# Kernel optimization log

Hardware: AMD Instinct MI355X
Metric: run time of the kernel (lower is better)

Reference implementation:

```python
import jax, jax.numpy as jnp
import numpy as np

N_NODES = 100000
N_EDGES = 1600000
IN_DIM = 128
OUT_DIM = 128


def setup_inputs() -> dict:
    key = jax.random.key(0)
    ks = jax.random.split(key, 8)
    x = jax.random.normal(ks[0], (N_NODES, IN_DIM), dtype=jnp.float32)
    one_hot_h = jax.random.normal(ks[1], (N_NODES, OUT_DIM), dtype=jnp.float32)
    # three candidate-op linear transforms (in_dim -> out_dim)
    W0 = jax.random.normal(ks[2], (IN_DIM, OUT_DIM), dtype=jnp.float32) * 0.05
    W1 = jax.random.normal(ks[3], (IN_DIM, OUT_DIM), dtype=jnp.float32) * 0.05
    W2 = jax.random.normal(ks[4], (IN_DIM, OUT_DIM), dtype=jnp.float32) * 0.05
    # sparse mask_matrix in COO form: out[r] += v * H[c]
    mask_rows = jax.random.randint(ks[5], (N_EDGES,), 0, N_NODES, dtype=jnp.int32)
    mask_cols = jax.random.randint(ks[6], (N_EDGES,), 0, N_NODES, dtype=jnp.int32)
    mask_vals = jax.random.uniform(ks[7], (N_EDGES,), dtype=jnp.float32)
    return {"x": x, "one_hot_h": one_hot_h, "W0": W0, "W1": W1, "W2": W2,
            "mask_rows": mask_rows, "mask_cols": mask_cols, "mask_vals": mask_vals}


def reference(x, one_hot_h, W0, W1, W2, mask_rows, mask_cols, mask_vals):
    # Original: sum_k spmm(mask_matrix, op_k(x)) + spmm(mask_matrix, one_hot_h).
    # spmm is linear, so summing per-op outputs pre-aggregation is exact and
    # fuses K spmm launches into one sparse aggregation pass.
    H = x @ W0 + x @ W1 + x @ W2 + one_hot_h              # [N, out_dim]
    gathered = mask_vals[:, None] * H[mask_cols]          # [E, out_dim]
    out = jax.ops.segment_sum(gathered, mask_rows, num_segments=x.shape[0])
    return out
```

## Files before the change

kernel.cpp:

```cpp
#include <hip/hip_runtime.h>
#include <hip/hip_bf16.h>

#define N_NODES 100000
#define N_EDGES 1600000
#define DIM 128

#define NBIN 512
#define RPP  196
#define PCAP 4096
#define P1_BLOCKS 512
#define CHUNK (N_EDGES / P1_BLOCKS)
#define GEMM_BLOCKS 1563

typedef unsigned int uint_t;
typedef unsigned short ushort_t;
typedef float f32x4 __attribute__((ext_vector_type(4)));
typedef __bf16 bf16x8 __attribute__((ext_vector_type(8)));

__device__ inline uint_t f2bf(float f) {
    uint_t u = __float_as_uint(f);
    return (u + 0x7FFFu + ((u >> 16) & 1u)) >> 16;
}
__device__ inline float bf2f(uint_t lo16) { return __uint_as_float(lo16 << 16); }

__global__ __launch_bounds__(256) void wt_init(const float* __restrict__ W0,
                                               const float* __restrict__ W1,
                                               const float* __restrict__ W2,
                                               ushort_t* __restrict__ WT,
                                               int* __restrict__ psize) {
    if (blockIdx.x == 64) {
        int i = threadIdx.x;
        if (i < NBIN / 2) { ((int2*)psize)[i] = make_int2(0, 0); }
        return;
    }
    int i = blockIdx.x * 256 + threadIdx.x;
    int m = i & 127, k = i >> 7;
    float s = W0[k * DIM + m] + W1[k * DIM + m] + W2[k * DIM + m];
    WT[m * DIM + k] = (ushort_t)f2bf(s);
}

#define GROWS 64
#define XSTR 136

__global__ __launch_bounds__(256) void fused_p1_gemm(
        const int* __restrict__ rows, const int* __restrict__ cols,
        const float* __restrict__ vals, int* __restrict__ psize,
        long long* __restrict__ slab,
        const float* __restrict__ x, const float* __restrict__ oh,
        const ushort_t* __restrict__ WT, uint_t* __restrict__ H16) {
    __shared__ __align__(16) char smem[8192 + CHUNK * 8 + CHUNK * 4];

    int role, idx;
    if (blockIdx.x < 2048) {
        int g = blockIdx.x >> 2, sb = blockIdx.x & 3;
        if (sb == 3) { role = 1; idx = g; }
        else         { role = 0; idx = g * 3 + sb; }
    } else {
        role = 0; idx = 1536 + (int)(blockIdx.x - 2048);
    }
    int t = threadIdx.x;

    if (role == 1) {
        int* hist   = (int*)smem;
        int* binoff = hist + NBIN;
        int* resv   = binoff + NBIN;
        int* curs   = resv + NBIN;
        long long* ebuf = (long long*)(smem + 8192);
        int* edest  = (int*)(smem + 8192 + CHUNK * 8);

        int e0 = idx * CHUNK;

        for (int i = t; i < NBIN; i += 256) hist[i] = 0;
        __syncthreads();

        for (int i = t; i < CHUNK; i += 256) {
            int r = rows[e0 + i];
            atomicAdd(&hist[r / RPP], 1);
        }
        __syncthreads();

        if (t < 64) {
            int b = t * 8;
            int v[8]; int s = 0;
#pragma unroll
            for (int k = 0; k < 8; ++k) { v[k] = hist[b + k]; s += v[k]; }
            int incl = s;
#pragma unroll
            for (int d = 1; d < 64; d <<= 1) {
                int o = __shfl_up(incl, d, 64);
                if (t >= d) incl += o;
            }
            int run = incl - s;
#pragma unroll
            for (int k = 0; k < 8; ++k) { binoff[b + k] = run; run += v[k]; }
        }
        __syncthreads();

        for (int i = t; i < NBIN; i += 256) {
            int len = hist[i];
            int r = (len > 0) ? atomicAdd(&psize[i], len) : 0;
            resv[i] = i * PCAP + r;
            curs[i] = binoff[i];
        }
        __syncthreads();

        for (int i = t; i < CHUNK; i += 256) {
            int   r = rows[e0 + i];
            int   c = cols[e0 + i];
            float v = vals[e0 + i];
            int b  = r / RPP;
            int lr = r - b * RPP;
            int pos = atomicAdd(&curs[b], 1);
            uint_t key = ((uint_t)lr << 17) | (uint_t)c;
            ebuf[pos]  = ((long long)__float_as_int(v) << 32) | (long long)key;
            edest[pos] = resv[b] + (pos - binoff[b]);
        }
        __syncthreads();

        for (int i = t; i < CHUNK; i += 256)
            slab[edest[i]] = ebuf[i];
    } else {
        ushort_t* xs = (ushort_t*)smem;

        int wv = t >> 6, l = t & 63;
        int lr = l & 15, kg = l >> 4;
        int lrow = wv * 16 + lr;
        long long base_row = (long long)idx * GROWS;
        long long hr = base_row + lrow;

        const f32x4* xg = (const f32x4*)x;
#pragma unroll
        for (int i = 0; i < 8; ++i) {
            int g = t + i * 256;
            int row = g >> 5, c4 = g & 31;
            long long sr = base_row + row; if (sr >= N_NODES) sr = N_NODES - 1;
            f32x4 v = __builtin_nontemporal_load(xg + sr * 32 + c4);
            ushort_t* d = &xs[row * XSTR + c4 * 4];
            d[0] = (ushort_t)f2bf(v.x); d[1] = (ushort_t)f2bf(v.y);
            d[2] = (ushort_t)f2bf(v.z); d[3] = (ushort_t)f2bf(v.w);
        }
        __syncthreads();

        f32x4 acc[8] = {};
#pragma unroll
        for (int s = 0; s < 4; ++s) {
            bf16x8 b = *(const bf16x8*)&xs[lrow * XSTR + s * 32 + kg * 8];
#pragma unroll
            for (int mt = 0; mt < 8; ++mt) {
                bf16x8 a = *(const bf16x8*)&WT[(mt * 16 + lr) * DIM + s * 32 + kg * 8];
                acc[mt] = __builtin_amdgcn_mfma_f32_16x16x32_bf16(a, b, acc[mt], 0, 0, 0);
            }
        }
        __syncthreads();

        const f32x4* og = (const f32x4*)oh;
#pragma unroll
        for (int i = 0; i < 8; ++i) {
            int g = t + i * 256;
            int row = g >> 5, c4 = g & 31;
            long long sr = base_row + row; if (sr >= N_NODES) sr = N_NODES - 1;
            f32x4 v = __builtin_nontemporal_load(og + sr * 32 + c4);
            ushort_t* d = &xs[row * XSTR + c4 * 4];
            d[0] = (ushort_t)f2bf(v.x); d[1] = (ushort_t)f2bf(v.y);
            d[2] = (ushort_t)f2bf(v.z); d[3] = (ushort_t)f2bf(v.w);
        }
        __syncthreads();

        if (hr < N_NODES) {
#pragma unroll
            for (int mt = 0; mt < 8; ++mt) {
                int c0 = mt * 16 + kg * 4;
                const uint_t* ow = (const uint_t*)&xs[lrow * XSTR + c0];
                uint_t w0 = ow[0], w1 = ow[1];
                float f0 = acc[mt].x + bf2f(w0 & 0xFFFFu);
                float f1 = acc[mt].y + bf2f(w0 >> 16);
                float f2 = acc[mt].z + bf2f(w1 & 0xFFFFu);
                float f3 = acc[mt].w + bf2f(w1 >> 16);
                uint2 pk;
                pk.x = f2bf(f0) | (f2bf(f1) << 16);
                pk.y = f2bf(f2) | (f2bf(f3) << 16);
                *(uint2*)&H16[(size_t)hr * (DIM / 2) + c0 / 2] = pk;
            }
        }
    }
}

__global__ __launch_bounds__(256) void pass2_sort(
        const long long* __restrict__ slab, const int* __restrict__ psize,
        int* __restrict__ off, long long* __restrict__ csr) {
    __shared__ int pb[NBIN + 1];
    __shared__ int cnt[RPP + 1];
    __shared__ int loff[RPP + 1];
    __shared__ int curs[RPP];
    __shared__ long long ebuf[PCAP];

    int p = blockIdx.x, t = threadIdx.x;

    if (t < 64) {
        int b = t * 8;
        int v[8]; int s = 0;
#pragma unroll
        for (int k = 0; k < 8; ++k) { v[k] = min(psize[b + k], PCAP); s += v[k]; }
        int incl = s;
#pragma unroll
        for (int d = 1; d < 64; d <<= 1) {
            int o = __shfl_up(incl, d, 64);
            if (t >= d) incl += o;
        }
        int run = incl - s;
#pragma unroll
        for (int k = 0; k < 8; ++k) { pb[b + k] = run; run += v[k]; }
        if (t == 63) pb[NBIN] = incl;
    }
    for (int i = t; i < RPP + 1; i += 256) cnt[i] = 0;
    __syncthreads();

    int n = min(psize[p], PCAP);
    int base = pb[p];
    int rlo = p * RPP;
    int nrows = N_NODES - rlo;
    if (nrows > RPP) nrows = RPP;
    if (nrows < 0) nrows = 0;
    const long long* seg = slab + (long long)p * PCAP;

    if (p == NBIN - 1 && t == 0) off[N_NODES] = pb[NBIN];

    for (int i = t; i < n; i += 256) {
        long long ev = __builtin_nontemporal_load(&seg[i]);
        ebuf[i] = ev;
        uint_t key = (uint_t)(ev & 0xFFFFFFFFll);
        atomicAdd(&cnt[key >> 17], 1);
    }
    __syncthreads();

    if (t < 64) {
        int b4 = t * 4;
        int v[4]; int s = 0;
#pragma unroll
        for (int k = 0; k < 4; ++k) {
            int idx = b4 + k;
            v[k] = (idx < RPP) ? cnt[idx] : 0;
            s += v[k];
        }
        int incl = s;
#pragma unroll
        for (int d = 1; d < 64; d <<= 1) {
            int o = __shfl_up(incl, d, 64);
            if (t >= d) incl += o;
        }
        int run = incl - s;
#pragma unroll
        for (int k = 0; k < 4; ++k) {
            int idx = b4 + k;
            if (idx < RPP) loff[idx] = run;
            run += v[k];
        }
    }
    __syncthreads();

    for (int i = t; i < nrows; i += 256) {
        curs[i] = loff[i];
        off[rlo + i] = base + loff[i];
    }
    __syncthreads();

    for (int i = t; i < n; i += 256) {
        long long ev = ebuf[i];
        uint_t key = (uint_t)(ev & 0xFFFFFFFFll);
        int lr = key >> 17;
        uint_t c = key & 0x1FFFFu;
        int pos = atomicAdd(&curs[lr], 1);
        csr[base + pos] = (long long)(((unsigned long long)ev & 0xFFFFFFFF00000000ull) | c);
    }
}

__global__ __launch_bounds__(256) void gather_kernel(const uint_t* __restrict__ H16,
                                                     const int* __restrict__ off,
                                                     const long long* __restrict__ csr,
                                                     float* __restrict__ out) {
    int tid  = threadIdx.x;
    int wave = tid >> 6;
    int lane = tid & 63;
    int grp  = lane >> 4;
    int il   = lane & 15;
    int wid  = blockIdx.x * 16 + wave * 4 + grp;

    int s = off[wid], e = off[wid + 1];
    float acc[8] = {};

#define ACC8(h, v)                                                            \
    acc[0] += (v) * bf2f((h).x & 0xFFFFu); acc[1] += (v) * bf2f((h).x >> 16); \
    acc[2] += (v) * bf2f((h).y & 0xFFFFu); acc[3] += (v) * bf2f((h).y >> 16); \
    acc[4] += (v) * bf2f((h).z & 0xFFFFu); acc[5] += (v) * bf2f((h).z >> 16); \
    acc[6] += (v) * bf2f((h).w & 0xFFFFu); acc[7] += (v) * bf2f((h).w >> 16);

    int p = s;
    for (; p + 3 < e; p += 4) {
        long long cv0 = __builtin_nontemporal_load(&csr[p]);
        long long cv1 = __builtin_nontemporal_load(&csr[p + 1]);
        long long cv2 = __builtin_nontemporal_load(&csr[p + 2]);
        long long cv3 = __builtin_nontemporal_load(&csr[p + 3]);
        uint4 h0 = *(const uint4*)&H16[(long long)(int)(cv0 & 0x1FFFF) * (DIM / 2) + il * 4];
        uint4 h1 = *(const uint4*)&H16[(long long)(int)(cv1 & 0x1FFFF) * (DIM / 2) + il * 4];
        uint4 h2 = *(const uint4*)&H16[(long long)(int)(cv2 & 0x1FFFF) * (DIM / 2) + il * 4];
        uint4 h3 = *(const uint4*)&H16[(long long)(int)(cv3 & 0x1FFFF) * (DIM / 2) + il * 4];
        float v0 = __int_as_float((int)(cv0 >> 32));
        float v1 = __int_as_float((int)(cv1 >> 32));
        float v2 = __int_as_float((int)(cv2 >> 32));
        float v3 = __int_as_float((int)(cv3 >> 32));
        ACC8(h0, v0) ACC8(h1, v1) ACC8(h2, v2) ACC8(h3, v3)
    }
    for (; p < e; ++p) {
        long long cv = __builtin_nontemporal_load(&csr[p]);
        float v = __int_as_float((int)(cv >> 32));
        uint4 h = *(const uint4*)&H16[(long long)(int)(cv & 0x1FFFF) * (DIM / 2) + il * 4];
        ACC8(h, v)
    }
#undef ACC8

    float* op = &out[(long long)wid * DIM + il * 8];
    f32x4 o0 = {acc[0], acc[1], acc[2], acc[3]};
    f32x4 o1 = {acc[4], acc[5], acc[6], acc[7]};
    __builtin_nontemporal_store(o0, (f32x4*)op);
    __builtin_nontemporal_store(o1, (f32x4*)(op + 4));
}

extern "C" void kernel_launch(void* const* d_in, const int* in_sizes, int n_in,
                              void* d_out, int out_size, void* d_ws, size_t ws_size,
                              hipStream_t stream) {
    const float* x    = (const float*)d_in[0];
    const float* oh   = (const float*)d_in[1];
    const float* W0   = (const float*)d_in[2];
    const float* W1   = (const float*)d_in[3];
    const float* W2   = (const float*)d_in[4];
    const int*   rows = (const int*)d_in[5];
    const int*   cols = (const int*)d_in[6];
    const float* vals = (const float*)d_in[7];
    float* out = (float*)d_out;

    char* p = (char*)d_ws;
    size_t oW    = 0;
    size_t oH    = oW + 64 * 1024;
    size_t oOff  = oH + (size_t)N_NODES * DIM * 2;
    size_t oPs   = oOff + (size_t)(N_NODES + 32) * 4;
    size_t oSlab = oPs + 4096;
    size_t oCsr  = oSlab + (size_t)NBIN * PCAP * 8;

    ushort_t*  WT    = (ushort_t*)(p + oW);
    uint_t*    H16   = (uint_t*)(p + oH);
    int*       off   = (int*)(p + oOff);
    int*       psize = (int*)(p + oPs);
    long long* slab  = (long long*)(p + oSlab);
    long long* csr   = (long long*)(p + oCsr);

    wt_init<<<65, 256, 0, stream>>>(W0, W1, W2, WT, psize);
    fused_p1_gemm<<<2075, 256, 0, stream>>>(rows, cols, vals, psize, slab,
                                            x, oh, WT, H16);
    pass2_sort<<<NBIN, 256, 0, stream>>>(slab, psize, off, csr);
    gather_kernel<<<N_NODES / 16, 256, 0, stream>>>(H16, off, csr, out);
}
```

Baseline: 151.3 us.

## Split GEMM across pass1 and pass2 kernels to overlap with bucket sort

The dense GEMM that builds H is split in two halves. One half is interleaved with pass-1 edge binning in the first fused kernel, and the other half is interleaved with the pass-2 per-bin sort in a new second fused kernel. This lets the memory-bound sort phases share the GPU with compute work, so the standalone pass2 launch no longer runs alone. The cost is larger shared memory in the second kernel, since pass2 buffers now live in a shared char array, which could limit occupancy.

```diff
diff --git a/kernel.cpp b/kernel.cpp
--- a/kernel.cpp
+++ b/kernel.cpp
@@ -10,7 +10,10 @@
 #define PCAP 4096
 #define P1_BLOCKS 512
 #define CHUNK (N_EDGES / P1_BLOCKS)
-#define GEMM_BLOCKS 1563
+
+#define GEMM_TOTAL 1563
+#define GEMM_A 782
+#define GEMM_B 781
 
 typedef unsigned int uint_t;
 typedef unsigned short ushort_t;
@@ -30,7 +33,7 @@
                                                int* __restrict__ psize) {
     if (blockIdx.x == 64) {
         int i = threadIdx.x;
-        if (i < NBIN / 2) { ((int2*)psize)[i] = make_int2(0, 0); }
+        if (i < NBIN / 2) ((int2*)psize)[i] = make_int2(0, 0);
         return;
     }
     int i = blockIdx.x * 256 + threadIdx.x;
@@ -42,159 +45,153 @@
 #define GROWS 64
 #define XSTR 136
 
-__global__ __launch_bounds__(256) void fused_p1_gemm(
-        const int* __restrict__ rows, const int* __restrict__ cols,
-        const float* __restrict__ vals, int* __restrict__ psize,
-        long long* __restrict__ slab,
-        const float* __restrict__ x, const float* __restrict__ oh,
-        const ushort_t* __restrict__ WT, uint_t* __restrict__ H16) {
-    __shared__ __align__(16) char smem[8192 + CHUNK * 8 + CHUNK * 4];
-
-    int role, idx;
-    if (blockIdx.x < 2048) {
-        int g = blockIdx.x >> 2, sb = blockIdx.x & 3;
-        if (sb == 3) { role = 1; idx = g; }
-        else         { role = 0; idx = g * 3 + sb; }
-    } else {
-        role = 0; idx = 1536 + (int)(blockIdx.x - 2048);
-    }
-    int t = threadIdx.x;
-
-    if (role == 1) {
-        int* hist   = (int*)smem;
-        int* binoff = hist + NBIN;
-        int* resv   = binoff + NBIN;
-        int* curs   = resv + NBIN;
-        long long* ebuf = (long long*)(smem + 8192);
-        int* edest  = (int*)(smem + 8192 + CHUNK * 8);
-
-        int e0 = idx * CHUNK;
-
-        for (int i = t; i < NBIN; i += 256) hist[i] = 0;
-        __syncthreads();
-
-        for (int i = t; i < CHUNK; i += 256) {
-            int r = rows[e0 + i];
-            atomicAdd(&hist[r / RPP], 1);
-        }
-        __syncthreads();
-
-        if (t < 64) {
-            int b = t * 8;
-            int v[8]; int s = 0;
-#pragma unroll
-            for (int k = 0; k < 8; ++k) { v[k] = hist[b + k]; s += v[k]; }
-            int incl = s;
-#pragma unroll
-            for (int d = 1; d < 64; d <<= 1) {
-                int o = __shfl_up(incl, d, 64);
-                if (t >= d) incl += o;
-            }
-            int run = incl - s;
-#pragma unroll
-            for (int k = 0; k < 8; ++k) { binoff[b + k] = run; run += v[k]; }
-        }
-        __syncthreads();
-
-        for (int i = t; i < NBIN; i += 256) {
-            int len = hist[i];
-            int r = (len > 0) ? atomicAdd(&psize[i], len) : 0;
-            resv[i] = i * PCAP + r;
-            curs[i] = binoff[i];
-        }
-        __syncthreads();
-
-        for (int i = t; i < CHUNK; i += 256) {
-            int   r = rows[e0 + i];
-            int   c = cols[e0 + i];
-            float v = vals[e0 + i];
-            int b  = r / RPP;
-            int lr = r - b * RPP;
-            int pos = atomicAdd(&curs[b], 1);
-            uint_t key = ((uint_t)lr << 17) | (uint_t)c;
-            ebuf[pos]  = ((long long)__float_as_int(v) << 32) | (long long)key;
-            edest[pos] = resv[b] + (pos - binoff[b]);
-        }
-        __syncthreads();
-
-        for (int i = t; i < CHUNK; i += 256)
-            slab[edest[i]] = ebuf[i];
-    } else {
-        ushort_t* xs = (ushort_t*)smem;
-
-        int wv = t >> 6, l = t & 63;
-        int lr = l & 15, kg = l >> 4;
-        int lrow = wv * 16 + lr;
-        long long base_row = (long long)idx * GROWS;
-        long long hr = base_row + lrow;
-
-        const f32x4* xg = (const f32x4*)x;
-#pragma unroll
-        for (int i = 0; i < 8; ++i) {
-            int g = t + i * 256;
-            int row = g >> 5, c4 = g & 31;
-            long long sr = base_row + row; if (sr >= N_NODES) sr = N_NODES - 1;
-            f32x4 v = __builtin_nontemporal_load(xg + sr * 32 + c4);
-            ushort_t* d = &xs[row * XSTR + c4 * 4];
-            d[0] = (ushort_t)f2bf(v.x); d[1] = (ushort_t)f2bf(v.y);
-            d[2] = (ushort_t)f2bf(v.z); d[3] = (ushort_t)f2bf(v.w);
-        }
-        __syncthreads();
-
-        f32x4 acc[8] = {};
-#pragma unroll
-        for (int s = 0; s < 4; ++s) {
-            bf16x8 b = *(const bf16x8*)&xs[lrow * XSTR + s * 32 + kg * 8];
-#pragma unroll
-            for (int mt = 0; mt < 8; ++mt) {
-                bf16x8 a = *(const bf16x8*)&WT[(mt * 16 + lr) * DIM + s * 32 + kg * 8];
-                acc[mt] = __builtin_amdgcn_mfma_f32_16x16x32_bf16(a, b, acc[mt], 0, 0, 0);
-            }
-        }
-        __syncthreads();
-
-        const f32x4* og = (const f32x4*)oh;
-#pragma unroll
-        for (int i = 0; i < 8; ++i) {
-            int g = t + i * 256;
-            int row = g >> 5, c4 = g & 31;
-            long long sr = base_row + row; if (sr >= N_NODES) sr = N_NODES - 1;
-            f32x4 v = __builtin_nontemporal_load(og + sr * 32 + c4);
-            ushort_t* d = &xs[row * XSTR + c4 * 4];
-            d[0] = (ushort_t)f2bf(v.x); d[1] = (ushort_t)f2bf(v.y);
-            d[2] = (ushort_t)f2bf(v.z); d[3] = (ushort_t)f2bf(v.w);
-        }
-        __syncthreads();
-
-        if (hr < N_NODES) {
-#pragma unroll
-            for (int mt = 0; mt < 8; ++mt) {
-                int c0 = mt * 16 + kg * 4;
-                const uint_t* ow = (const uint_t*)&xs[lrow * XSTR + c0];
-                uint_t w0 = ow[0], w1 = ow[1];
-                float f0 = acc[mt].x + bf2f(w0 & 0xFFFFu);
-                float f1 = acc[mt].y + bf2f(w0 >> 16);
-                float f2 = acc[mt].z + bf2f(w1 & 0xFFFFu);
-                float f3 = acc[mt].w + bf2f(w1 >> 16);
-                uint2 pk;
-                pk.x = f2bf(f0) | (f2bf(f1) << 16);
-                pk.y = f2bf(f2) | (f2bf(f3) << 16);
-                *(uint2*)&H16[(size_t)hr * (DIM / 2) + c0 / 2] = pk;
-            }
-        }
-    }
-}
-
-__global__ __launch_bounds__(256) void pass2_sort(
-        const long long* __restrict__ slab, const int* __restrict__ psize,
-        int* __restrict__ off, long long* __restrict__ csr) {
-    __shared__ int pb[NBIN + 1];
-    __shared__ int cnt[RPP + 1];
-    __shared__ int loff[RPP + 1];
-    __shared__ int curs[RPP];
-    __shared__ long long ebuf[PCAP];
-
-    int p = blockIdx.x, t = threadIdx.x;
+__device__ __forceinline__ void gemm_body(int idx, int t, char* smem,
+                                          const float* __restrict__ x,
+                                          const float* __restrict__ oh,
+                                          const ushort_t* __restrict__ WT,
+                                          uint_t* __restrict__ H16) {
+    ushort_t* xs = (ushort_t*)smem;
+
+    int wv = t >> 6, l = t & 63;
+    int lr = l & 15, kg = l >> 4;
+    int lrow = wv * 16 + lr;
+    long long base_row = (long long)idx * GROWS;
+    long long hr = base_row + lrow;
+
+    const f32x4* xg = (const f32x4*)x;
+#pragma unroll
+    for (int i = 0; i < 8; ++i) {
+        int g = t + i * 256;
+        int row = g >> 5, c4 = g & 31;
+        long long sr = base_row + row; if (sr >= N_NODES) sr = N_NODES - 1;
+        f32x4 v = __builtin_nontemporal_load(xg + sr * 32 + c4);
+        ushort_t* d = &xs[row * XSTR + c4 * 4];
+        d[0] = (ushort_t)f2bf(v.x); d[1] = (ushort_t)f2bf(v.y);
+        d[2] = (ushort_t)f2bf(v.z); d[3] = (ushort_t)f2bf(v.w);
+    }
+    __syncthreads();
+
+    f32x4 acc[8] = {};
+#pragma unroll
+    for (int s = 0; s < 4; ++s) {
+        bf16x8 b = *(const bf16x8*)&xs[lrow * XSTR + s * 32 + kg * 8];
+#pragma unroll
+        for (int mt = 0; mt < 8; ++mt) {
+            bf16x8 a = *(const bf16x8*)&WT[(mt * 16 + lr) * DIM + s * 32 + kg * 8];
+            acc[mt] = __builtin_amdgcn_mfma_f32_16x16x32_bf16(a, b, acc[mt], 0, 0, 0);
+        }
+    }
+    __syncthreads();
+
+    const f32x4* og = (const f32x4*)oh;
+#pragma unroll
+    for (int i = 0; i < 8; ++i) {
+        int g = t + i * 256;
+        int row = g >> 5, c4 = g & 31;
+        long long sr = base_row + row; if (sr >= N_NODES) sr = N_NODES - 1;
+        f32x4 v = __builtin_nontemporal_load(og + sr * 32 + c4);
+        ushort_t* d = &xs[row * XSTR + c4 * 4];
+        d[0] = (ushort_t)f2bf(v.x); d[1] = (ushort_t)f2bf(v.y);
+        d[2] = (ushort_t)f2bf(v.z); d[3] = (ushort_t)f2bf(v.w);
+    }
+    __syncthreads();
+
+    if (hr < N_NODES) {
+#pragma unroll
+        for (int mt = 0; mt < 8; ++mt) {
+            int c0 = mt * 16 + kg * 4;
+            const uint_t* ow = (const uint_t*)&xs[lrow * XSTR + c0];
+            uint_t w0 = ow[0], w1 = ow[1];
+            float f0 = acc[mt].x + bf2f(w0 & 0xFFFFu);
+            float f1 = acc[mt].y + bf2f(w0 >> 16);
+            float f2 = acc[mt].z + bf2f(w1 & 0xFFFFu);
+            float f3 = acc[mt].w + bf2f(w1 >> 16);
+            uint2 pk;
+            pk.x = f2bf(f0) | (f2bf(f1) << 16);
+            pk.y = f2bf(f2) | (f2bf(f3) << 16);
+            *(uint2*)&H16[(size_t)hr * (DIM / 2) + c0 / 2] = pk;
+        }
+    }
+}
+
+__device__ __forceinline__ void pass1_body(int idx, int t, char* smem,
+                                           const int* __restrict__ rows,
+                                           const int* __restrict__ cols,
+                                           const float* __restrict__ vals,
+                                           int* __restrict__ psize,
+                                           long long* __restrict__ slab) {
+    int* hist   = (int*)smem;
+    int* binoff = hist + NBIN;
+    int* resv   = binoff + NBIN;
+    int* curs   = resv + NBIN;
+    long long* ebuf = (long long*)(smem + 8192);
+    int* edest  = (int*)(smem + 8192 + CHUNK * 8);
+
+    int e0 = idx * CHUNK;
+
+    for (int i = t; i < NBIN; i += 256) hist[i] = 0;
+    __syncthreads();
+
+    for (int i = t; i < CHUNK; i += 256) {
+        int r = rows[e0 + i];
+        atomicAdd(&hist[r / RPP], 1);
+    }
+    __syncthreads();
+
+    if (t < 64) {
+        int b = t * 8;
+        int v[8]; int s = 0;
+#pragma unroll
+        for (int k = 0; k < 8; ++k) { v[k] = hist[b + k]; s += v[k]; }
+        int incl = s;
+#pragma unroll
+        for (int d = 1; d < 64; d <<= 1) {
+            int o = __shfl_up(incl, d, 64);
+            if (t >= d) incl += o;
+        }
+        int run = incl - s;
+#pragma unroll
+        for (int k = 0; k < 8; ++k) { binoff[b + k] = run; run += v[k]; }
+    }
+    __syncthreads();
+
+    for (int i = t; i < NBIN; i += 256) {
+        int len = hist[i];
+        int r = (len > 0) ? atomicAdd(&psize[i], len) : 0;
+        resv[i] = i * PCAP + r;
+        curs[i] = binoff[i];
+    }
+    __syncthreads();
+
+    for (int i = t; i < CHUNK; i += 256) {
+        int   r = rows[e0 + i];
+        int   c = cols[e0 + i];
+        float v = vals[e0 + i];
+        int b  = r / RPP;
+        int lr = r - b * RPP;
+        int pos = atomicAdd(&curs[b], 1);
+        uint_t key = ((uint_t)lr << 17) | (uint_t)c;
+        ebuf[pos]  = ((long long)__float_as_int(v) << 32) | (long long)key;
+        edest[pos] = resv[b] + (pos - binoff[b]);
+    }
+    __syncthreads();
+
+    for (int i = t; i < CHUNK; i += 256)
+        slab[edest[i]] = ebuf[i];
+}
+
+#define SM_EBUF 4416
+
+__device__ __forceinline__ void pass2_body(int p, int t, char* smem,
+                                           const long long* __restrict__ slab,
+                                           const int* __restrict__ psize,
+                                           int* __restrict__ off,
+                                           long long* __restrict__ csr) {
+    int* pb   = (int*)smem;
+    int* cnt  = pb + NBIN + 1;
+    int* loff = cnt + RPP + 1;
+    int* curs = loff + RPP + 1;
+    long long* ebuf = (long long*)(smem + SM_EBUF);
 
     if (t < 64) {
         int b = t * 8;
@@ -238,8 +235,8 @@
         int v[4]; int s = 0;
 #pragma unroll
         for (int k = 0; k < 4; ++k) {
-            int idx = b4 + k;
-            v[k] = (idx < RPP) ? cnt[idx] : 0;
+            int idx2 = b4 + k;
+            v[k] = (idx2 < RPP) ? cnt[idx2] : 0;
             s += v[k];
         }
         int incl = s;
@@ -251,8 +248,8 @@
         int run = incl - s;
 #pragma unroll
         for (int k = 0; k < 4; ++k) {
-            int idx = b4 + k;
-            if (idx < RPP) loff[idx] = run;
+            int idx2 = b4 + k;
+            if (idx2 < RPP) loff[idx2] = run;
             run += v[k];
         }
     }
@@ -271,6 +268,39 @@
         uint_t c = key & 0x1FFFFu;
         int pos = atomicAdd(&curs[lr], 1);
         csr[base + pos] = (long long)(((unsigned long long)ev & 0xFFFFFFFF00000000ull) | c);
+    }
+}
+
+__global__ __launch_bounds__(256) void fused_p1_gemmA(
+        const int* __restrict__ rows, const int* __restrict__ cols,
+        const float* __restrict__ vals, int* __restrict__ psize,
+        long long* __restrict__ slab,
+        const float* __restrict__ x, const float* __restrict__ oh,
+        const ushort_t* __restrict__ WT, uint_t* __restrict__ H16) {
+    __shared__ __align__(16) char smem[8192 + CHUNK * 8 + CHUNK * 4];
+    int bid = blockIdx.x, t = threadIdx.x;
+    if (bid < 1280) {
+        int g = bid / 5, sb = bid - g * 5;
+        if (sb < 2) pass1_body(g * 2 + sb, t, smem, rows, cols, vals, psize, slab);
+        else        gemm_body(g * 3 + (sb - 2), t, smem, x, oh, WT, H16);
+    } else {
+        gemm_body(768 + (bid - 1280), t, smem, x, oh, WT, H16);
+    }
+}
+
+__global__ __launch_bounds__(256) void fused_p2_gemmB(
+        const long long* __restrict__ slab, const int* __restrict__ psize,
+        int* __restrict__ off, long long* __restrict__ csr,
+        const float* __restrict__ x, const float* __restrict__ oh,
+        const ushort_t* __restrict__ WT, uint_t* __restrict__ H16) {
+    __shared__ __align__(16) char smem[SM_EBUF + PCAP * 8];
+    int bid = blockIdx.x, t = threadIdx.x;
+    if (bid < 1280) {
+        int g = bid / 5, sb = bid - g * 5;
+        if (sb < 2) pass2_body(g * 2 + sb, t, smem, slab, psize, off, csr);
+        else        gemm_body(GEMM_A + g * 3 + (sb - 2), t, smem, x, oh, WT, H16);
+    } else {
+        gemm_body(GEMM_A + 768 + (bid - 1280), t, smem, x, oh, WT, H16);
     }
 }
 
@@ -354,8 +384,9 @@
     long long* csr   = (long long*)(p + oCsr);
 
     wt_init<<<65, 256, 0, stream>>>(W0, W1, W2, WT, psize);
-    fused_p1_gemm<<<2075, 256, 0, stream>>>(rows, cols, vals, psize, slab,
-                                            x, oh, WT, H16);
-    pass2_sort<<<NBIN, 256, 0, stream>>>(slab, psize, off, csr);
+    fused_p1_gemmA<<<1294, 256, 0, stream>>>(rows, cols, vals, psize, slab,
+                                             x, oh, WT, H16);
+    fused_p2_gemmB<<<1293, 256, 0, stream>>>(slab, psize, off, csr,
+                                             x, oh, WT, H16);
     gather_kernel<<<N_NODES / 16, 256, 0, stream>>>(H16, off, csr, out);
 }
```

New measurement: 155.3 us. +2.6%, slower.
